# Performance work log

Measured on AMD Instinct MI355X. Metric: run time of the kernel, lower is better.

The kernel has to match this reference:

```python
import jax, jax.numpy as jnp
import numpy as np

B, F, T = 256, 64, 1024  # batch, num_frequencies, trailing columns; state dim = 2F = 128


def setup_inputs() -> dict:
    key = jax.random.key(0)
    k1, k2, k3, k4 = jax.random.split(key, 4)
    x = jax.random.normal(k1, (B, 2 * F, T), dtype=jnp.float32)
    # positive dts so amp**dt and 2*pi/|dt| in the repo are well-behaved
    delta_t = jax.random.uniform(k2, (B,), dtype=jnp.float32, minval=0.5, maxval=2.0)
    # learned params: amplitudes init'd to 1.0, frequencies ~ U(0, 2*pi) in the torch code;
    # perturb amplitudes slightly so the amp**dt path is exercised
    amplitudes = jax.random.uniform(k3, (F,), dtype=jnp.float32, minval=0.7, maxval=1.3)
    frequencies = jax.random.uniform(k4, (F,), dtype=jnp.float32, minval=0.0, maxval=2.0 * np.pi)
    return {"x": x, "delta_t": delta_t, "amplitudes": amplitudes, "frequencies": frequencies}


def reference(x, delta_t, amplitudes, frequencies):
    # Per-sample Jordan rotation matrix is block-diagonal with 2x2 blocks
    #   a^dt * [[cos(w*dt), -sin(w*dt)], [sin(w*dt), cos(w*dt)]]
    # Apply blocks directly instead of materializing the sparse [2F,2F] matrix.
    Bn = x.shape[0]
    Fn = amplitudes.shape[0]
    a = amplitudes[None, :] ** delta_t[:, None]          # [B, F]
    ang = frequencies[None, :] * delta_t[:, None]        # [B, F]
    c = a * jnp.cos(ang)                                 # [B, F]
    s = a * jnp.sin(ang)                                 # [B, F]
    xr = x.reshape(Bn, Fn, 2, -1)                        # [B, F, 2, T]
    x0, x1 = xr[:, :, 0], xr[:, :, 1]                    # [B, F, T]
    out0 = c[..., None] * x0 - s[..., None] * x1
    out1 = s[..., None] * x0 + c[..., None] * x1
    return jnp.stack([out0, out1], axis=2).reshape(x.shape)
```

## Files before the change

kernel.cpp:

```cpp
#include <hip/hip_runtime.h>


constexpr int Bn = 256;
constexpr int Fn = 64;
constexpr int Tn = 1024;
constexpr int CHUNKS = 4;

typedef float v4f __attribute__((ext_vector_type(4)));

__global__ __launch_bounds__(256) void koopman_kernel(
    const float* __restrict__ x,
    const float* __restrict__ delta_t,
    const float* __restrict__ amplitudes,
    const float* __restrict__ frequencies,
    float* __restrict__ out) {
    const int t   = threadIdx.x;
    const int bf0 = blockIdx.x * CHUNKS;

    const v4f* __restrict__ xp = reinterpret_cast<const v4f*>(x)
                               + (size_t)bf0 * (2 * Tn / 4);
    v4f*       __restrict__ op = reinterpret_cast<v4f*>(out)
                               + (size_t)bf0 * (2 * Tn / 4);

    v4f v0[CHUNKS], v1[CHUNKS];
#pragma unroll
    for (int j = 0; j < CHUNKS; ++j) {
        v0[j] = __builtin_nontemporal_load(&xp[j * 512 + t]);
        v1[j] = __builtin_nontemporal_load(&xp[j * 512 + 256 + t]);
    }

    float cc[CHUNKS], ss[CHUNKS];
#pragma unroll
    for (int j = 0; j < CHUNKS; ++j) {
        const int bf = bf0 + j;
        const int b  = bf >> 6;
        const int f  = bf & 63;
        const float d = delta_t[b];
        const float a = __builtin_amdgcn_exp2f(d * __builtin_amdgcn_logf(amplitudes[f]));
        const float rev = (frequencies[f] * d) * 0.15915494309189535f;
        ss[j] = a * __builtin_amdgcn_sinf(rev);
        cc[j] = a * __builtin_amdgcn_cosf(rev);
    }

#pragma unroll
    for (int j = 0; j < CHUNKS; ++j) {
        const v4f r0 = cc[j] * v0[j] - ss[j] * v1[j];
        const v4f r1 = ss[j] * v0[j] + cc[j] * v1[j];
        __builtin_nontemporal_store(r0, &op[j * 512 + t]);
        __builtin_nontemporal_store(r1, &op[j * 512 + 256 + t]);
    }
}

extern "C" void kernel_launch(void* const* d_in, const int* in_sizes, int n_in,
                              void* d_out, int out_size, void* d_ws, size_t ws_size,
                              hipStream_t stream) {
    const float* x    = (const float*)d_in[0];
    const float* dt   = (const float*)d_in[1];
    const float* amp  = (const float*)d_in[2];
    const float* freq = (const float*)d_in[3];
    float* out = (float*)d_out;

    static_assert((Bn * Fn) % CHUNKS == 0, "grid divisibility");
    koopman_kernel<<<dim3(Bn * Fn / CHUNKS), dim3(256), 0, stream>>>(x, dt, amp, freq, out);
}
```

Measured before the change: 222.7 us.

## Software-pipeline row loop with next-row prefetch and fewer, longer-lived blocks

Each block now processes eight rows in a loop, prefetching the next row's inputs while computing and storing the current row, instead of loading four rows up front. The grid is halved and input loads become regular rather than nontemporal. The intent is to overlap load latency with compute and stores while reducing block launch overhead, at the cost of fewer outstanding loads per thread.

```diff
diff --git a/kernel.cpp b/kernel.cpp
--- a/kernel.cpp
+++ b/kernel.cpp
@@ -4,7 +4,8 @@
 constexpr int Bn = 256;
 constexpr int Fn = 64;
 constexpr int Tn = 1024;
-constexpr int CHUNKS = 4;
+constexpr int ITERS = 8;
+constexpr int GRID  = Bn * Fn / ITERS;
 
 typedef float v4f __attribute__((ext_vector_type(4)));
 
@@ -14,40 +15,41 @@
     const float* __restrict__ amplitudes,
     const float* __restrict__ frequencies,
     float* __restrict__ out) {
-    const int t   = threadIdx.x;
-    const int bf0 = blockIdx.x * CHUNKS;
+    const int t      = threadIdx.x;
+    const int bfBase = blockIdx.x * ITERS;
 
     const v4f* __restrict__ xp = reinterpret_cast<const v4f*>(x)
-                               + (size_t)bf0 * (2 * Tn / 4);
+                               + (size_t)bfBase * 512;
     v4f*       __restrict__ op = reinterpret_cast<v4f*>(out)
-                               + (size_t)bf0 * (2 * Tn / 4);
+                               + (size_t)bfBase * 512;
 
-    v4f v0[CHUNKS], v1[CHUNKS];
-#pragma unroll
-    for (int j = 0; j < CHUNKS; ++j) {
-        v0[j] = __builtin_nontemporal_load(&xp[j * 512 + t]);
-        v1[j] = __builtin_nontemporal_load(&xp[j * 512 + 256 + t]);
-    }
+    v4f a0 = xp[t];
+    v4f a1 = xp[t + 256];
 
-    float cc[CHUNKS], ss[CHUNKS];
-#pragma unroll
-    for (int j = 0; j < CHUNKS; ++j) {
-        const int bf = bf0 + j;
+#pragma unroll 2
+    for (int j = 0; j < ITERS; ++j) {
+        v4f n0, n1;
+        if (j + 1 < ITERS) {
+            n0 = xp[(j + 1) * 512 + t];
+            n1 = xp[(j + 1) * 512 + 256 + t];
+        }
+
+        const int bf = bfBase + j;
         const int b  = bf >> 6;
         const int f  = bf & 63;
         const float d = delta_t[b];
         const float a = __builtin_amdgcn_exp2f(d * __builtin_amdgcn_logf(amplitudes[f]));
         const float rev = (frequencies[f] * d) * 0.15915494309189535f;
-        ss[j] = a * __builtin_amdgcn_sinf(rev);
-        cc[j] = a * __builtin_amdgcn_cosf(rev);
-    }
+        const float s = a * __builtin_amdgcn_sinf(rev);
+        const float c = a * __builtin_amdgcn_cosf(rev);
 
-#pragma unroll
-    for (int j = 0; j < CHUNKS; ++j) {
-        const v4f r0 = cc[j] * v0[j] - ss[j] * v1[j];
-        const v4f r1 = ss[j] * v0[j] + cc[j] * v1[j];
+        const v4f r0 = c * a0 - s * a1;
+        const v4f r1 = s * a0 + c * a1;
         __builtin_nontemporal_store(r0, &op[j * 512 + t]);
         __builtin_nontemporal_store(r1, &op[j * 512 + 256 + t]);
+
+        a0 = n0;
+        a1 = n1;
     }
 }
 
@@ -60,6 +62,6 @@
     const float* freq = (const float*)d_in[3];
     float* out = (float*)d_out;
 
-    static_assert((Bn * Fn) % CHUNKS == 0, "grid divisibility");
-    koopman_kernel<<<dim3(Bn * Fn / CHUNKS), dim3(256), 0, stream>>>(x, dt, amp, freq, out);
+    static_assert((Bn * Fn) % ITERS == 0, "grid divisibility");
+    koopman_kernel<<<dim3(GRID), dim3(256), 0, stream>>>(x, dt, amp, freq, out);
 }
```

New measurement: 239.1 us. +7.3%, slower.
